# Performance work log

Hardware: AMD Instinct MI355X
Metric: run time of the kernel (lower is better)

Reference implementation:

```python
import jax, jax.numpy as jnp
import numpy as np

N_USERS = 100000
N_ITEMS = 50000
N_NODES = N_USERS + N_ITEMS
N_EDGES = 10000000
DIM = 64
N_LAYERS = 3


def setup_inputs() -> dict:
    key = jax.random.key(0)
    k1, k2, k3, k4, k5, k6, k7 = jax.random.split(key, 7)
    users = jax.random.randint(k1, (8192,), 0, N_USERS, dtype=jnp.int64 if jax.config.jax_enable_x64 else jnp.int32)
    items = jax.random.randint(k2, (8192,), 0, N_ITEMS, dtype=users.dtype)
    edge_src = jax.random.randint(k3, (N_EDGES,), 0, N_NODES, dtype=users.dtype)
    edge_dst = jax.random.randint(k4, (N_EDGES,), 0, N_NODES, dtype=users.dtype)
    edge_vals = jax.random.uniform(k5, (N_EDGES,), dtype=jnp.float32)
    user_emb = 0.1 * jax.random.normal(k6, (N_USERS, DIM), dtype=jnp.float32)
    item_emb = 0.1 * jax.random.normal(k7, (N_ITEMS, DIM), dtype=jnp.float32)
    return {"users": users, "items": items, "edge_src": edge_src,
            "edge_dst": edge_dst, "edge_vals": edge_vals,
            "user_emb": user_emb, "item_emb": item_emb}


def _spmm(edge_src, edge_dst, edge_vals, x):
    # y[dst] += vals * x[src]  (COO SpMM, edge-parallel)
    msgs = edge_vals[:, None] * x[edge_src]          # [E, D]
    return jax.ops.segment_sum(msgs, edge_dst, num_segments=N_NODES)


def _compute(edge_src, edge_dst, edge_vals, user_emb, item_emb):
    all_emds = jnp.concatenate([user_emb, item_emb], axis=0)  # [N, D]
    acc = all_emds
    cur = all_emds
    for _ in range(N_LAYERS):
        cur = _spmm(edge_src, edge_dst, edge_vals, cur)
        acc = acc + cur
    lgn_out = acc / jnp.asarray(N_LAYERS + 1, dtype=acc.dtype)  # mean over stacked layers
    return lgn_out[:N_USERS], lgn_out[N_USERS:]


def reference(users, items, edge_src, edge_dst, edge_vals, user_emb, item_emb):
    all_users, all_items = _compute(edge_src, edge_dst, edge_vals, user_emb, item_emb)
    users_embs = all_users[users]   # [B, D]
    items_embs = all_items[items]   # [B, D]
    gamma = jnp.sum(users_embs * items_embs, axis=1)  # [B]
    return gamma
```

## Files before the change

kernel.cpp:

```cpp
#include <hip/hip_runtime.h>

#define DIM 64
#define BROWS 512
#define LNB 512
#define TILE 8192
#define PMAXE 40960

typedef unsigned short bf16_t;

typedef int      iv4 __attribute__((ext_vector_type(4)));
typedef float    fv4 __attribute__((ext_vector_type(4)));
typedef unsigned uv4 __attribute__((ext_vector_type(4)));

__device__ __forceinline__ float bf2f_lo(unsigned u) {
    return __uint_as_float(u << 16);
}
__device__ __forceinline__ float bf2f_hi(unsigned u) {
    return __uint_as_float(u & 0xFFFF0000u);
}
__device__ __forceinline__ unsigned short f2bf(float f) {
    unsigned u = __float_as_uint(f);
    u += 0x7FFFu + ((u >> 16) & 1u);
    return (unsigned short)(u >> 16);
}
__device__ __forceinline__ unsigned pack2(float lo, float hi) {
    return (unsigned)f2bf(lo) | ((unsigned)f2bf(hi) << 16);
}

__device__ __forceinline__ unsigned enc_val14(float v) {
    float s = v * 16384.f + 0.5f;
    int u = (int)s;
    if (u > 16383) u = 16383;
    if (u < 0) u = 0;
    return (unsigned)u;
}
#define DEC_VAL14(p) ((float)((p) >> 18) * 6.103515625e-05f)
#define SRC_OF(p)    ((p) & 0x3FFFFu)

__global__ void build_xb(const float4* __restrict__ ue, const float4* __restrict__ ie,
                         ushort4* __restrict__ xb, long nU4, long total4) {
    long i = (long)blockIdx.x * blockDim.x + threadIdx.x;
    if (i >= total4) return;
    float4 v = (i < nU4) ? ue[i] : ie[i - nU4];
    ushort4 o;
    o.x = f2bf(v.x); o.y = f2bf(v.y); o.z = f2bf(v.z); o.w = f2bf(v.w);
    xb[i] = o;
}

__global__ void gather_accum_f32_2(const int* __restrict__ users, const int* __restrict__ items,
                                   const float* __restrict__ ue, const float* __restrict__ ie,
                                   float* __restrict__ accU, float* __restrict__ accI, int B) {
    long gid = (long)blockIdx.x * blockDim.x + threadIdx.x;
    int lane = (int)(gid & 15);
    long g = gid >> 4;
    if (g >= 2 * (long)B) return;
    const int* idx = (g < B) ? users : items;
    const float* x = (g < B) ? ue : ie;
    float* acc = (g < B) ? accU : accI;
    long b = (g < B) ? g : g - B;
    long node = (long)idx[b];
    float4 r = ((const float4*)(x + node * DIM))[lane];
    float4* a = (float4*)(acc + b * DIM) + lane;
    float4 av = *a;
    av.x += r.x; av.y += r.y; av.z += r.z; av.w += r.w;
    *a = av;
}

__global__ void gather_accum_bf16_2(const int* __restrict__ users, const int* __restrict__ items,
                                    int nU, const bf16_t* __restrict__ xb,
                                    float* __restrict__ accU, float* __restrict__ accI, int B) {
    long gid = (long)blockIdx.x * blockDim.x + threadIdx.x;
    int lane = (int)(gid & 7);
    long g = gid >> 3;
    if (g >= 2 * (long)B) return;
    long b;
    long node;
    float* acc;
    if (g < B) { b = g;     node = (long)users[b];      acc = accU; }
    else       { b = g - B; node = (long)items[b] + nU; acc = accI; }
    int4 r = *(const int4*)(xb + node * DIM + lane * 8);
    float4* ap = (float4*)(acc + b * DIM + lane * 8);
    float4 a0 = ap[0], a1 = ap[1];
    a0.x += bf2f_lo(r.x); a0.y += bf2f_hi(r.x);
    a0.z += bf2f_lo(r.y); a0.w += bf2f_hi(r.y);
    a1.x += bf2f_lo(r.z); a1.y += bf2f_hi(r.z);
    a1.z += bf2f_lo(r.w); a1.w += bf2f_hi(r.w);
    ap[0] = a0; ap[1] = a1;
}

__global__ void dot_pairs(const float* __restrict__ aU, const float* __restrict__ aI,
                          float* __restrict__ out, int B) {
    long gid = (long)blockIdx.x * blockDim.x + threadIdx.x;
    int lane = (int)(gid & 15);
    long b = gid >> 4;
    if (b >= B) return;
    float4 u = ((const float4*)(aU + b * DIM))[lane];
    float4 v = ((const float4*)(aI + b * DIM))[lane];
    float s = u.x * v.x + u.y * v.y + u.z * v.z + u.w * v.w;
    s += __shfl_xor(s, 1);
    s += __shfl_xor(s, 2);
    s += __shfl_xor(s, 4);
    s += __shfl_xor(s, 8);
    if (lane == 0) out[b] = s * (1.0f / 16.0f);
}

__global__ __launch_bounds__(1024) void bucket_hist(const int* __restrict__ edst,
                                                    int* __restrict__ bcnt, int E, int NB) {
    __shared__ int h[LNB];
    for (int i = threadIdx.x; i < NB; i += 1024) h[i] = 0;
    __syncthreads();
    int base = blockIdx.x * TILE;
    int end = base + TILE; if (end > E) end = E;
    int e = base + threadIdx.x * 4;
    for (; e + 3 < end; e += 4096) {
        iv4 d = __builtin_nontemporal_load((const iv4*)(edst + e));
        atomicAdd(&h[d.x >> 9], 1);
        atomicAdd(&h[d.y >> 9], 1);
        atomicAdd(&h[d.z >> 9], 1);
        atomicAdd(&h[d.w >> 9], 1);
    }
    for (; e < end; ++e)
        atomicAdd(&h[edst[e] >> 9], 1);
    __syncthreads();
    for (int i = threadIdx.x; i < NB; i += 1024)
        if (h[i]) atomicAdd(&bcnt[i], h[i]);
}

__global__ void scan_buckets(const int* __restrict__ bcnt, int* __restrict__ bptr,
                             int* __restrict__ bcur, int NB) {
    __shared__ int tmp[1024];
    int i = threadIdx.x;
    int v = (i < NB) ? bcnt[i] : 0;
    tmp[i] = v;
    __syncthreads();
    for (int off = 1; off < 1024; off <<= 1) {
        int t = (i >= off) ? tmp[i - off] : 0;
        __syncthreads();
        tmp[i] += t;
        __syncthreads();
    }
    if (i < NB) {
        int inc = tmp[i];
        bptr[i + 1] = inc;
        bcur[i] = inc - v;
        if (i == 0) bptr[0] = 0;
    }
}

__global__ void scan_block(const int* __restrict__ cnt, int* __restrict__ out,
                           int* __restrict__ blockSums, int n) {
    __shared__ int tmp[256];
    int i = blockIdx.x * 256 + threadIdx.x;
    int v = (i < n) ? cnt[i] : 0;
    tmp[threadIdx.x] = v;
    __syncthreads();
    for (int off = 1; off < 256; off <<= 1) {
        int t = (threadIdx.x >= off) ? tmp[threadIdx.x - off] : 0;
        __syncthreads();
        tmp[threadIdx.x] += t;
        __syncthreads();
    }
    if (i < n) out[i] = tmp[threadIdx.x];
    if (threadIdx.x == 255) blockSums[blockIdx.x] = tmp[255];
}

__global__ void scan_sums(int* __restrict__ blockSums, int nb) {
    __shared__ int tmp[1024];
    int i = threadIdx.x;
    tmp[i] = (i < nb) ? blockSums[i] : 0;
    __syncthreads();
    for (int off = 1; off < 1024; off <<= 1) {
        int t = (i >= off) ? tmp[i - off] : 0;
        __syncthreads();
        tmp[i] += t;
        __syncthreads();
    }
    if (i < nb) blockSums[i] = (i > 0) ? tmp[i - 1] : 0;
}

__global__ void scan_finalize(const int* __restrict__ cnt, const int* __restrict__ blockSums,
                              int* __restrict__ outp, int* __restrict__ start, int n) {
    int i = blockIdx.x * 256 + threadIdx.x;
    if (i >= n) return;
    int inc = outp[i + 1] + blockSums[blockIdx.x];
    outp[i + 1] = inc;
    start[i] = inc - cnt[i];
    if (i == 0) outp[0] = 0;
}

__global__ __launch_bounds__(1024) void bucket_scatter(
        const int* __restrict__ esrc, const int* __restrict__ edst,
        const float* __restrict__ evals, int* __restrict__ bcur,
        unsigned* __restrict__ tmpw, unsigned short* __restrict__ tmpd,
        int E, int NB) {
    __shared__ int h[LNB];
    __shared__ int cb[LNB];
    __shared__ int lofs[LNB];
    __shared__ unsigned sw[TILE];
    __shared__ unsigned short sd[TILE];
    const int tid = threadIdx.x;
    for (int i = tid; i < NB; i += 1024) h[i] = 0;
    __syncthreads();
    int base = blockIdx.x * TILE;
    int end = base + TILE; if (end > E) end = E;
    int e = base + tid * 4;
    for (; e + 3 < end; e += 4096) {
        iv4 d = __builtin_nontemporal_load((const iv4*)(edst + e));
        atomicAdd(&h[d.x >> 9], 1);
        atomicAdd(&h[d.y >> 9], 1);
        atomicAdd(&h[d.z >> 9], 1);
        atomicAdd(&h[d.w >> 9], 1);
    }
    for (; e < end; ++e)
        atomicAdd(&h[edst[e] >> 9], 1);
    __syncthreads();
    if (tid < LNB) lofs[tid] = (tid < NB) ? h[tid] : 0;
    __syncthreads();
    for (int off = 1; off < LNB; off <<= 1) {
        int t = (tid < LNB && tid >= off) ? lofs[tid - off] : 0;
        __syncthreads();
        if (tid < LNB) lofs[tid] += t;
        __syncthreads();
    }
    if (tid < NB) {
        int c = h[tid];
        cb[tid] = c ? atomicAdd(&bcur[tid], c) : 0;
    }
    __syncthreads();
    if (tid < NB) h[tid] = 0;
    __syncthreads();
    e = base + tid * 4;
    for (; e + 3 < end; e += 4096) {
        iv4 d4 = __builtin_nontemporal_load((const iv4*)(edst + e));
        iv4 s4 = __builtin_nontemporal_load((const iv4*)(esrc + e));
        fv4 v4 = __builtin_nontemporal_load((const fv4*)(evals + e));
        #pragma unroll
        for (int k = 0; k < 4; ++k) {
            int d = (k == 0) ? d4.x : (k == 1) ? d4.y : (k == 2) ? d4.z : d4.w;
            int s = (k == 0) ? s4.x : (k == 1) ? s4.y : (k == 2) ? s4.z : s4.w;
            float v = (k == 0) ? v4.x : (k == 1) ? v4.y : (k == 2) ? v4.z : v4.w;
            int b = d >> 9;
            int r = atomicAdd(&h[b], 1);
            int idx = (b ? lofs[b - 1] : 0) + r;
            sw[idx] = (unsigned)s | (enc_val14(v) << 18);
            sd[idx] = (unsigned short)(d & 511);
        }
    }
    for (; e < end; ++e) {
        int d = edst[e];
        int s = esrc[e];
        float v = evals[e];
        int b = d >> 9;
        int r = atomicAdd(&h[b], 1);
        int idx = (b ? lofs[b - 1] : 0) + r;
        sw[idx] = (unsigned)s | (enc_val14(v) << 18);
        sd[idx] = (unsigned short)(d & 511);
    }
    __syncthreads();
    int wid = tid >> 6;
    int lane = tid & 63;
    for (int b = wid; b < NB; b += 16) {
        int c = h[b];
        if (!c) continue;
        int sb = b ? lofs[b - 1] : 0;
        int gb = cb[b];
        for (int k = lane; k < c; k += 64) {
            tmpw[gb + k] = sw[sb + k];
            tmpd[gb + k] = sd[sb + k];
        }
    }
}

__device__ __forceinline__ void csr_hist_scan_rowptr(
        const unsigned short* __restrict__ tmpd, int beg, int end,
        int* lcnt, int* lofs, int* __restrict__ rowptr, int rbase, int N, int b, int NB) {
    const int T = 1024;
    if (threadIdx.x < BROWS) lcnt[threadIdx.x] = 0;
    __syncthreads();
    for (int e = beg + threadIdx.x; e < end; e += T) {
        int dl = __builtin_nontemporal_load(tmpd + e);
        atomicAdd(&lcnt[dl], 1);
    }
    __syncthreads();
    if (threadIdx.x < BROWS) lofs[threadIdx.x] = lcnt[threadIdx.x];
    __syncthreads();
    for (int off = 1; off < BROWS; off <<= 1) {
        int t = (threadIdx.x < BROWS && threadIdx.x >= off) ? lofs[threadIdx.x - off] : 0;
        __syncthreads();
        if (threadIdx.x < BROWS) lofs[threadIdx.x] += t;
        __syncthreads();
    }
    if (threadIdx.x < BROWS) {
        int r = rbase + threadIdx.x;
        if (r < N) rowptr[r] = beg + (threadIdx.x ? lofs[threadIdx.x - 1] : 0);
    }
    if (b == NB - 1 && threadIdx.x == 0) rowptr[N] = end;
    if (threadIdx.x < BROWS) lcnt[threadIdx.x] = 0;
    __syncthreads();
}

__global__ __launch_bounds__(1024) void csr_from_buckets_perm(
        const int* __restrict__ bptr, const unsigned* __restrict__ tmpw,
        const unsigned short* __restrict__ tmpd,
        unsigned* __restrict__ pairs, int* __restrict__ rowptr, int N, int NB) {
    extern __shared__ unsigned short perm[];
    __shared__ int lcnt[BROWS];
    __shared__ int lofs[BROWS];
    const int T = 1024;
    int b = blockIdx.x;
    int beg = bptr[b], end = bptr[b + 1];
    int cnt = end - beg;
    csr_hist_scan_rowptr(tmpd, beg, end, lcnt, lofs, rowptr, b * BROWS, N, b, NB);
    if (cnt <= PMAXE) {
        for (int e = beg + threadIdx.x; e < end; e += T) {
            int dl = __builtin_nontemporal_load(tmpd + e);
            int r = atomicAdd(&lcnt[dl], 1);
            int j = (dl ? lofs[dl - 1] : 0) + r;
            perm[j] = (unsigned short)(e - beg);
        }
        __syncthreads();
        for (int j = threadIdx.x; j < cnt; j += T)
            pairs[beg + j] = tmpw[beg + (int)perm[j]];
    } else {
        for (int e = beg + threadIdx.x; e < end; e += T) {
            unsigned w = tmpw[e];
            int dl = tmpd[e];
            int r = atomicAdd(&lcnt[dl], 1);
            pairs[beg + (dl ? lofs[dl - 1] : 0) + r] = w;
        }
    }
}

__global__ void csr_from_buckets(const int* __restrict__ bptr, const unsigned* __restrict__ tmpw,
                                 const unsigned short* __restrict__ tmpd,
                                 unsigned* __restrict__ pairs, int* __restrict__ rowptr,
                                 int N, int NB) {
    __shared__ int lcnt[BROWS];
    __shared__ int lofs[BROWS];
    const int T = 1024;
    int b = blockIdx.x;
    int beg = bptr[b], end = bptr[b + 1];
    csr_hist_scan_rowptr(tmpd, beg, end, lcnt, lofs, rowptr, b * BROWS, N, b, NB);
    for (int e = beg + threadIdx.x; e < end; e += T) {
        unsigned w = __builtin_nontemporal_load(tmpw + e);
        int dl = __builtin_nontemporal_load(tmpd + e);
        int r = atomicAdd(&lcnt[dl], 1);
        int basep = beg + (dl ? lofs[dl - 1] : 0);
        pairs[basep + r] = w;
    }
}

__global__ void count_deg(const int* __restrict__ dst, int* __restrict__ cnt, int E) {
    int e = blockIdx.x * blockDim.x + threadIdx.x;
    if (e >= E) return;
    atomicAdd(&cnt[dst[e]], 1);
}

__global__ void csr_fill(const int* __restrict__ src, const int* __restrict__ dst,
                         const float* __restrict__ vals, int* __restrict__ cursor,
                         unsigned* __restrict__ pairs, int E) {
    int e = blockIdx.x * blockDim.x + threadIdx.x;
    if (e >= E) return;
    int d = dst[e];
    int pos = atomicAdd(&cursor[d], 1);
    pairs[pos] = (unsigned)src[e] | (enc_val14(vals[e]) << 18);
}

template<int U>
__device__ __forceinline__ void spmm_body(const unsigned* pw, const bf16_t* __restrict__ xb,
                                          int lane, float* a) {
    int4 rr[U];
    #pragma unroll
    for (int k = 0; k < U; ++k)
        rr[k] = *(const int4*)(xb + (long)SRC_OF(pw[k]) * DIM + lane * 8);
    #pragma unroll
    for (int k = 0; k < U; ++k) {
        float v = DEC_VAL14(pw[k]);
        a[0] += v * bf2f_lo(rr[k].x); a[1] += v * bf2f_hi(rr[k].x);
        a[2] += v * bf2f_lo(rr[k].y); a[3] += v * bf2f_hi(rr[k].y);
        a[4] += v * bf2f_lo(rr[k].z); a[5] += v * bf2f_hi(rr[k].z);
        a[6] += v * bf2f_lo(rr[k].w); a[7] += v * bf2f_hi(rr[k].w);
    }
}

__device__ __forceinline__ void spmm_row(const unsigned* __restrict__ pairs, int beg, int end,
                                         const bf16_t* __restrict__ xb, int lane, float* a) {
    int e = beg;
    for (; e < end && (e & 3); ++e) {
        unsigned p = __builtin_nontemporal_load(pairs + e);
        spmm_body<1>(&p, xb, lane, a);
    }
    for (; e + 7 < end; e += 8) {
        uv4 w0 = __builtin_nontemporal_load((const uv4*)(pairs + e));
        uv4 w1 = __builtin_nontemporal_load((const uv4*)(pairs + e + 4));
        unsigned pw[8] = {w0.x, w0.y, w0.z, w0.w, w1.x, w1.y, w1.z, w1.w};
        spmm_body<8>(pw, xb, lane, a);
    }
    if (e + 3 < end) {
        uv4 w0 = __builtin_nontemporal_load((const uv4*)(pairs + e));
        unsigned pw[4] = {w0.x, w0.y, w0.z, w0.w};
        spmm_body<4>(pw, xb, lane, a);
        e += 4;
    }
    for (; e < end; ++e) {
        unsigned p = __builtin_nontemporal_load(pairs + e);
        spmm_body<1>(&p, xb, lane, a);
    }
}

__global__ void spmm_pull_bf16(const int* __restrict__ rowptr, const unsigned* __restrict__ pairs,
                               const bf16_t* __restrict__ xb, bf16_t* __restrict__ yb, int Nrows) {
    long gid = (long)blockIdx.x * blockDim.x + threadIdx.x;
    int lane = (int)(gid & 7);
    long r = gid >> 3;
    if (r >= Nrows) return;
    int beg = rowptr[r];
    int end = rowptr[r + 1];
    float a[8] = {0.f, 0.f, 0.f, 0.f, 0.f, 0.f, 0.f, 0.f};
    spmm_row(pairs, beg, end, xb, lane, a);
    int4 o;
    o.x = (int)pack2(a[0], a[1]);
    o.y = (int)pack2(a[2], a[3]);
    o.z = (int)pack2(a[4], a[5]);
    o.w = (int)pack2(a[6], a[7]);
    *(int4*)(yb + r * DIM + lane * 8) = o;
}

__global__ void spmm_rows_accum_fused(const int* __restrict__ users, const int* __restrict__ items,
                                      int nU, const int* __restrict__ rowptr,
                                      const unsigned* __restrict__ pairs, const bf16_t* __restrict__ xb,
                                      float* __restrict__ accU, float* __restrict__ accI, int B) {
    long gid = (long)blockIdx.x * blockDim.x + threadIdx.x;
    int lane = (int)(gid & 7);
    long g = gid >> 3;
    if (g >= 2 * (long)B) return;
    long b;
    long row;
    float* acc;
    if (g < B) { b = g;     row = (long)users[b];      acc = accU; }
    else       { b = g - B; row = (long)items[b] + nU; acc = accI; }
    int beg = rowptr[row];
    int end = rowptr[row + 1];
    int4 rs = *(const int4*)(xb + row * DIM + lane * 8);
    float a[8] = { bf2f_lo(rs.x), bf2f_hi(rs.x), bf2f_lo(rs.y), bf2f_hi(rs.y),
                   bf2f_lo(rs.z), bf2f_hi(rs.z), bf2f_lo(rs.w), bf2f_hi(rs.w) };
    spmm_row(pairs, beg, end, xb, lane, a);
    float4* ap = (float4*)(acc + b * DIM + lane * 8);
    float4 x0 = ap[0], x1 = ap[1];
    x0.x += a[0]; x0.y += a[1]; x0.z += a[2]; x0.w += a[3];
    x1.x += a[4]; x1.y += a[5]; x1.z += a[6]; x1.w += a[7];
    ap[0] = x0; ap[1] = x1;
}

extern "C" void kernel_launch(void* const* d_in, const int* in_sizes, int n_in,
                              void* d_out, int out_size, void* d_ws, size_t ws_size,
                              hipStream_t stream) {
    const int*   users = (const int*)d_in[0];
    const int*   items = (const int*)d_in[1];
    const int*   esrc  = (const int*)d_in[2];
    const int*   edst  = (const int*)d_in[3];
    const float* evals = (const float*)d_in[4];
    const float* uemb  = (const float*)d_in[5];
    const float* iemb  = (const float*)d_in[6];

    const int B  = in_sizes[0];
    const int E  = in_sizes[2];
    const int nU = in_sizes[5] / DIM;
    const int nI = in_sizes[6] / DIM;
    const int N  = nU + nI;
    const int NB = (N + BROWS - 1) / BROWS;

    const int T = 256;
    float* gout = (float*)d_out;

    static const bool perm_ok = []() {
        return hipFuncSetAttribute(
                   reinterpret_cast<const void*>(csr_from_buckets_perm),
                   hipFuncAttributeMaxDynamicSharedMemorySize,
                   PMAXE * (int)sizeof(unsigned short)) == hipSuccess;
    }();

    char* p = (char*)d_ws;
    float*  accU  = (float*)p;          p += (size_t)B * DIM * 4;
    float*  accI  = (float*)p;          p += (size_t)B * DIM * 4;
    bf16_t* xbCur = (bf16_t*)p;         p += (size_t)N * DIM * 2;
    bf16_t* xbNxt = (bf16_t*)p;         p += (size_t)N * DIM * 2;
    int*    rowptr = (int*)p;           p += (size_t)(N + 1) * 4;
    int*    bcnt   = (int*)p;           p += (size_t)NB * 4;
    int*    bptr   = (int*)p;           p += (size_t)(NB + 1) * 4;
    int*    bcur   = (int*)p;           p += (size_t)NB * 4;
    int*    blockSums = (int*)p;        p += 1024 * 4;
    int*    cnt    = (int*)p;           p += (size_t)N * 4;
    int*    cursor = (int*)p;           p += (size_t)N * 4;
    p = (char*)(((size_t)p + 15) & ~(size_t)15);
    unsigned* pairs = (unsigned*)p;     p += (size_t)E * 4;
    p = (char*)(((size_t)p + 15) & ~(size_t)15);
    size_t need_fb = (size_t)(p - (char*)d_ws);
    unsigned* tmpw = (unsigned*)p;      p += (size_t)E * 4;
    p = (char*)(((size_t)p + 15) & ~(size_t)15);
    unsigned short* tmpd = (unsigned short*)p; p += (size_t)E * 2;
    size_t need_fast = (size_t)(p - (char*)d_ws);
    (void)need_fb;

    long total4 = (long)N * (DIM / 4);
    long nU4    = (long)nU * (DIM / 4);
    int gb32 = (int)(((long)B * 32 + T - 1) / T);
    int gb16 = (int)(((long)B * 16 + T - 1) / T);
    int eb = (E + T - 1) / T;

    hipMemsetAsync(accU, 0, (size_t)B * DIM * 2 * sizeof(float), stream);
    gather_accum_f32_2<<<gb32, T, 0, stream>>>(users, items, uemb, iemb, accU, accI, B);

    build_xb<<<(int)((total4 + T - 1) / T), T, 0, stream>>>(
        (const float4*)uemb, (const float4*)iemb, (ushort4*)xbCur, nU4, total4);

    if (ws_size >= need_fast && NB <= LNB && N <= (1 << 18)) {
        int tb = (E + TILE - 1) / TILE;
        hipMemsetAsync(bcnt, 0, (size_t)NB * sizeof(int), stream);
        bucket_hist<<<tb, 1024, 0, stream>>>(edst, bcnt, E, NB);
        scan_buckets<<<1, 1024, 0, stream>>>(bcnt, bptr, bcur, NB);
        bucket_scatter<<<tb, 1024, 0, stream>>>(esrc, edst, evals, bcur, tmpw, tmpd, E, NB);
        if (perm_ok) {
            csr_from_buckets_perm<<<NB, 1024, PMAXE * sizeof(unsigned short), stream>>>(
                bptr, tmpw, tmpd, pairs, rowptr, N, NB);
        } else {
            csr_from_buckets<<<NB, 1024, 0, stream>>>(bptr, tmpw, tmpd, pairs, rowptr, N, NB);
        }
    } else {
        hipMemsetAsync(cnt, 0, (size_t)N * sizeof(int), stream);
        count_deg<<<eb, T, 0, stream>>>(edst, cnt, E);
        int nbN = (N + 255) / 256;
        scan_block<<<nbN, 256, 0, stream>>>(cnt, rowptr + 1, blockSums, N);
        scan_sums<<<1, 1024, 0, stream>>>(blockSums, nbN);
        scan_finalize<<<nbN, 256, 0, stream>>>(cnt, blockSums, rowptr, cursor, N);
        csr_fill<<<eb, T, 0, stream>>>(esrc, edst, evals, cursor, pairs, E);
    }

    int pb8 = (int)(((long)N * 8 + T - 1) / T);
    spmm_pull_bf16<<<pb8, T, 0, stream>>>(rowptr, pairs, xbCur, xbNxt, N);
    gather_accum_bf16_2<<<gb16, T, 0, stream>>>(users, items, nU, xbNxt, accU, accI, B);
    spmm_pull_bf16<<<pb8, T, 0, stream>>>(rowptr, pairs, xbNxt, xbCur, N);

    spmm_rows_accum_fused<<<gb16, T, 0, stream>>>(users, items, nU, rowptr, pairs, xbCur,
                                                  accU, accI, B);

    dot_pairs<<<gb16, T, 0, stream>>>(accU, accI, gout, B);
}
```

Before: 753.3 us.

## Quantize node embeddings to int8 with per-row scale for SpMM gathers

```diff
diff --git a/kernel.cpp b/kernel.cpp
--- a/kernel.cpp
+++ b/kernel.cpp
@@ -11,21 +11,6 @@
 typedef int      iv4 __attribute__((ext_vector_type(4)));
 typedef float    fv4 __attribute__((ext_vector_type(4)));
 typedef unsigned uv4 __attribute__((ext_vector_type(4)));
-
-__device__ __forceinline__ float bf2f_lo(unsigned u) {
-    return __uint_as_float(u << 16);
-}
-__device__ __forceinline__ float bf2f_hi(unsigned u) {
-    return __uint_as_float(u & 0xFFFF0000u);
-}
-__device__ __forceinline__ unsigned short f2bf(float f) {
-    unsigned u = __float_as_uint(f);
-    u += 0x7FFFu + ((u >> 16) & 1u);
-    return (unsigned short)(u >> 16);
-}
-__device__ __forceinline__ unsigned pack2(float lo, float hi) {
-    return (unsigned)f2bf(lo) | ((unsigned)f2bf(hi) << 16);
-}
 
 __device__ __forceinline__ unsigned enc_val14(float v) {
     float s = v * 16384.f + 0.5f;
@@ -37,14 +22,56 @@
 #define DEC_VAL14(p) ((float)((p) >> 18) * 6.103515625e-05f)
 #define SRC_OF(p)    ((p) & 0x3FFFFu)
 
-__global__ void build_xb(const float4* __restrict__ ue, const float4* __restrict__ ie,
-                         ushort4* __restrict__ xb, long nU4, long total4) {
-    long i = (long)blockIdx.x * blockDim.x + threadIdx.x;
-    if (i >= total4) return;
-    float4 v = (i < nU4) ? ue[i] : ie[i - nU4];
-    ushort4 o;
-    o.x = f2bf(v.x); o.y = f2bf(v.y); o.z = f2bf(v.z); o.w = f2bf(v.w);
-    xb[i] = o;
+__device__ __forceinline__ void quant_store_row(const float* a, int lane,
+                                                unsigned char* __restrict__ xq,
+                                                float* __restrict__ sc, long row) {
+    float m = 0.f;
+    #pragma unroll
+    for (int k = 0; k < 8; ++k) m = fmaxf(m, fabsf(a[k]));
+    m = fmaxf(m, __shfl_xor(m, 1));
+    m = fmaxf(m, __shfl_xor(m, 2));
+    m = fmaxf(m, __shfl_xor(m, 4));
+    float inv = (m > 0.f) ? 127.f / m : 0.f;
+    unsigned w0 = 0, w1 = 0;
+    #pragma unroll
+    for (int k = 0; k < 4; ++k) {
+        int q = (int)rintf(a[k] * inv);
+        w0 |= ((unsigned)(q & 0xFF)) << (8 * k);
+    }
+    #pragma unroll
+    for (int k = 0; k < 4; ++k) {
+        int q = (int)rintf(a[4 + k] * inv);
+        w1 |= ((unsigned)(q & 0xFF)) << (8 * k);
+    }
+    uint2 o; o.x = w0; o.y = w1;
+    *(uint2*)(xq + row * DIM + lane * 8) = o;
+    if (lane == 0) sc[row] = m * (1.0f / 127.0f);
+}
+
+__device__ __forceinline__ void dec8_accum(uint2 r, float v, float* a) {
+    unsigned x = r.x, y = r.y;
+    a[0] += v * (float)(((int)(x << 24)) >> 24);
+    a[1] += v * (float)(((int)(x << 16)) >> 24);
+    a[2] += v * (float)(((int)(x <<  8)) >> 24);
+    a[3] += v * (float)(((int)x) >> 24);
+    a[4] += v * (float)(((int)(y << 24)) >> 24);
+    a[5] += v * (float)(((int)(y << 16)) >> 24);
+    a[6] += v * (float)(((int)(y <<  8)) >> 24);
+    a[7] += v * (float)(((int)y) >> 24);
+}
+
+__global__ void build_xb_q8(const float* __restrict__ ue, const float* __restrict__ ie,
+                            unsigned char* __restrict__ xq, float* __restrict__ sc,
+                            int nU, int N) {
+    long gid = (long)blockIdx.x * blockDim.x + threadIdx.x;
+    int lane = (int)(gid & 7);
+    long r = gid >> 3;
+    if (r >= N) return;
+    const float* srcp = (r < nU) ? (ue + r * DIM) : (ie + (r - nU) * DIM);
+    float4 f0 = ((const float4*)srcp)[lane * 2];
+    float4 f1 = ((const float4*)srcp)[lane * 2 + 1];
+    float a[8] = {f0.x, f0.y, f0.z, f0.w, f1.x, f1.y, f1.z, f1.w};
+    quant_store_row(a, lane, xq, sc, r);
 }
 
 __global__ void gather_accum_f32_2(const int* __restrict__ users, const int* __restrict__ items,
@@ -66,9 +93,10 @@
     *a = av;
 }
 
-__global__ void gather_accum_bf16_2(const int* __restrict__ users, const int* __restrict__ items,
-                                    int nU, const bf16_t* __restrict__ xb,
-                                    float* __restrict__ accU, float* __restrict__ accI, int B) {
+__global__ void gather_accum_q8_2(const int* __restrict__ users, const int* __restrict__ items,
+                                  int nU, const unsigned char* __restrict__ xq,
+                                  const float* __restrict__ xs,
+                                  float* __restrict__ accU, float* __restrict__ accI, int B) {
     long gid = (long)blockIdx.x * blockDim.x + threadIdx.x;
     int lane = (int)(gid & 7);
     long g = gid >> 3;
@@ -78,13 +106,14 @@
     float* acc;
     if (g < B) { b = g;     node = (long)users[b];      acc = accU; }
     else       { b = g - B; node = (long)items[b] + nU; acc = accI; }
-    int4 r = *(const int4*)(xb + node * DIM + lane * 8);
+    uint2 r = *(const uint2*)(xq + node * DIM + lane * 8);
+    float s = xs[node];
+    float a[8] = {0.f, 0.f, 0.f, 0.f, 0.f, 0.f, 0.f, 0.f};
+    dec8_accum(r, s, a);
     float4* ap = (float4*)(acc + b * DIM + lane * 8);
     float4 a0 = ap[0], a1 = ap[1];
-    a0.x += bf2f_lo(r.x); a0.y += bf2f_hi(r.x);
-    a0.z += bf2f_lo(r.y); a0.w += bf2f_hi(r.y);
-    a1.x += bf2f_lo(r.z); a1.y += bf2f_hi(r.z);
-    a1.z += bf2f_lo(r.w); a1.w += bf2f_hi(r.w);
+    a0.x += a[0]; a0.y += a[1]; a0.z += a[2]; a0.w += a[3];
+    a1.x += a[4]; a1.y += a[5]; a1.z += a[6]; a1.w += a[7];
     ap[0] = a0; ap[1] = a1;
 }
 
@@ -367,49 +396,51 @@
 }
 
 template<int U>
-__device__ __forceinline__ void spmm_body(const unsigned* pw, const bf16_t* __restrict__ xb,
-                                          int lane, float* a) {
-    int4 rr[U];
+__device__ __forceinline__ void spmm_body(const unsigned* pw,
+                                          const unsigned char* __restrict__ xq,
+                                          const float* __restrict__ xs, int lane, float* a) {
+    uint2 rr[U];
+    float vs[U];
+    #pragma unroll
+    for (int k = 0; k < U; ++k) {
+        long s = (long)SRC_OF(pw[k]);
+        rr[k] = *(const uint2*)(xq + s * DIM + lane * 8);
+        vs[k] = DEC_VAL14(pw[k]) * xs[s];
+    }
     #pragma unroll
     for (int k = 0; k < U; ++k)
-        rr[k] = *(const int4*)(xb + (long)SRC_OF(pw[k]) * DIM + lane * 8);
-    #pragma unroll
-    for (int k = 0; k < U; ++k) {
-        float v = DEC_VAL14(pw[k]);
-        a[0] += v * bf2f_lo(rr[k].x); a[1] += v * bf2f_hi(rr[k].x);
-        a[2] += v * bf2f_lo(rr[k].y); a[3] += v * bf2f_hi(rr[k].y);
-        a[4] += v * bf2f_lo(rr[k].z); a[5] += v * bf2f_hi(rr[k].z);
-        a[6] += v * bf2f_lo(rr[k].w); a[7] += v * bf2f_hi(rr[k].w);
-    }
+        dec8_accum(rr[k], vs[k], a);
 }
 
 __device__ __forceinline__ void spmm_row(const unsigned* __restrict__ pairs, int beg, int end,
-                                         const bf16_t* __restrict__ xb, int lane, float* a) {
+                                         const unsigned char* __restrict__ xq,
+                                         const float* __restrict__ xs, int lane, float* a) {
     int e = beg;
     for (; e < end && (e & 3); ++e) {
         unsigned p = __builtin_nontemporal_load(pairs + e);
-        spmm_body<1>(&p, xb, lane, a);
+        spmm_body<1>(&p, xq, xs, lane, a);
     }
     for (; e + 7 < end; e += 8) {
         uv4 w0 = __builtin_nontemporal_load((const uv4*)(pairs + e));
         uv4 w1 = __builtin_nontemporal_load((const uv4*)(pairs + e + 4));
         unsigned pw[8] = {w0.x, w0.y, w0.z, w0.w, w1.x, w1.y, w1.z, w1.w};
-        spmm_body<8>(pw, xb, lane, a);
+        spmm_body<8>(pw, xq, xs, lane, a);
     }
     if (e + 3 < end) {
         uv4 w0 = __builtin_nontemporal_load((const uv4*)(pairs + e));
         unsigned pw[4] = {w0.x, w0.y, w0.z, w0.w};
-        spmm_body<4>(pw, xb, lane, a);
+        spmm_body<4>(pw, xq, xs, lane, a);
         e += 4;
     }
     for (; e < end; ++e) {
         unsigned p = __builtin_nontemporal_load(pairs + e);
-        spmm_body<1>(&p, xb, lane, a);
-    }
-}
-
-__global__ void spmm_pull_bf16(const int* __restrict__ rowptr, const unsigned* __restrict__ pairs,
-                               const bf16_t* __restrict__ xb, bf16_t* __restrict__ yb, int Nrows) {
+        spmm_body<1>(&p, xq, xs, lane, a);
+    }
+}
+
+__global__ void spmm_pull_q8(const int* __restrict__ rowptr, const unsigned* __restrict__ pairs,
+                             const unsigned char* __restrict__ xq, const float* __restrict__ xs,
+                             unsigned char* __restrict__ yq, float* __restrict__ ys, int Nrows) {
     long gid = (long)blockIdx.x * blockDim.x + threadIdx.x;
     int lane = (int)(gid & 7);
     long r = gid >> 3;
@@ -417,18 +448,15 @@
     int beg = rowptr[r];
     int end = rowptr[r + 1];
     float a[8] = {0.f, 0.f, 0.f, 0.f, 0.f, 0.f, 0.f, 0.f};
-    spmm_row(pairs, beg, end, xb, lane, a);
-    int4 o;
-    o.x = (int)pack2(a[0], a[1]);
-    o.y = (int)pack2(a[2], a[3]);
-    o.z = (int)pack2(a[4], a[5]);
-    o.w = (int)pack2(a[6], a[7]);
-    *(int4*)(yb + r * DIM + lane * 8) = o;
+    spmm_row(pairs, beg, end, xq, xs, lane, a);
+    quant_store_row(a, lane, yq, ys, r);
 }
 
 __global__ void spmm_rows_accum_fused(const int* __restrict__ users, const int* __restrict__ items,
                                       int nU, const int* __restrict__ rowptr,
-                                      const unsigned* __restrict__ pairs, const bf16_t* __restrict__ xb,
+                                      const unsigned* __restrict__ pairs,
+                                      const unsigned char* __restrict__ xq,
+                                      const float* __restrict__ xs,
                                       float* __restrict__ accU, float* __restrict__ accI, int B) {
     long gid = (long)blockIdx.x * blockDim.x + threadIdx.x;
     int lane = (int)(gid & 7);
@@ -441,10 +469,10 @@
     else       { b = g - B; row = (long)items[b] + nU; acc = accI; }
     int beg = rowptr[row];
     int end = rowptr[row + 1];
-    int4 rs = *(const int4*)(xb + row * DIM + lane * 8);
-    float a[8] = { bf2f_lo(rs.x), bf2f_hi(rs.x), bf2f_lo(rs.y), bf2f_hi(rs.y),
-                   bf2f_lo(rs.z), bf2f_hi(rs.z), bf2f_lo(rs.w), bf2f_hi(rs.w) };
-    spmm_row(pairs, beg, end, xb, lane, a);
+    float a[8] = {0.f, 0.f, 0.f, 0.f, 0.f, 0.f, 0.f, 0.f};
+    uint2 rs = *(const uint2*)(xq + row * DIM + lane * 8);
+    dec8_accum(rs, xs[row], a);
+    spmm_row(pairs, beg, end, xq, xs, lane, a);
     float4* ap = (float4*)(acc + b * DIM + lane * 8);
     float4 x0 = ap[0], x1 = ap[1];
     x0.x += a[0]; x0.y += a[1]; x0.z += a[2]; x0.w += a[3];
@@ -483,8 +511,11 @@
     char* p = (char*)d_ws;
     float*  accU  = (float*)p;          p += (size_t)B * DIM * 4;
     float*  accI  = (float*)p;          p += (size_t)B * DIM * 4;
-    bf16_t* xbCur = (bf16_t*)p;         p += (size_t)N * DIM * 2;
-    bf16_t* xbNxt = (bf16_t*)p;         p += (size_t)N * DIM * 2;
+    unsigned char* xqCur = (unsigned char*)p;  p += (size_t)N * DIM;
+    unsigned char* xqNxt = (unsigned char*)p;  p += (size_t)N * DIM;
+    p = (char*)(((size_t)p + 15) & ~(size_t)15);
+    float*  scCur = (float*)p;          p += (size_t)N * 4;
+    float*  scNxt = (float*)p;          p += (size_t)N * 4;
     int*    rowptr = (int*)p;           p += (size_t)(N + 1) * 4;
     int*    bcnt   = (int*)p;           p += (size_t)NB * 4;
     int*    bptr   = (int*)p;           p += (size_t)(NB + 1) * 4;
@@ -502,8 +533,6 @@
     size_t need_fast = (size_t)(p - (char*)d_ws);
     (void)need_fb;
 
-    long total4 = (long)N * (DIM / 4);
-    long nU4    = (long)nU * (DIM / 4);
     int gb32 = (int)(((long)B * 32 + T - 1) / T);
     int gb16 = (int)(((long)B * 16 + T - 1) / T);
     int eb = (E + T - 1) / T;
@@ -511,8 +540,8 @@
     hipMemsetAsync(accU, 0, (size_t)B * DIM * 2 * sizeof(float), stream);
     gather_accum_f32_2<<<gb32, T, 0, stream>>>(users, items, uemb, iemb, accU, accI, B);
 
-    build_xb<<<(int)((total4 + T - 1) / T), T, 0, stream>>>(
-        (const float4*)uemb, (const float4*)iemb, (ushort4*)xbCur, nU4, total4);
+    int qb8 = (int)(((long)N * 8 + T - 1) / T);
+    build_xb_q8<<<qb8, T, 0, stream>>>(uemb, iemb, xqCur, scCur, nU, N);
 
     if (ws_size >= need_fast && NB <= LNB && N <= (1 << 18)) {
         int tb = (E + TILE - 1) / TILE;
@@ -537,12 +566,12 @@
     }
 
     int pb8 = (int)(((long)N * 8 + T - 1) / T);
-    spmm_pull_bf16<<<pb8, T, 0, stream>>>(rowptr, pairs, xbCur, xbNxt, N);
-    gather_accum_bf16_2<<<gb16, T, 0, stream>>>(users, items, nU, xbNxt, accU, accI, B);
-    spmm_pull_bf16<<<pb8, T, 0, stream>>>(rowptr, pairs, xbNxt, xbCur, N);
-
-    spmm_rows_accum_fused<<<gb16, T, 0, stream>>>(users, items, nU, rowptr, pairs, xbCur,
-                                                  accU, accI, B);
+    spmm_pull_q8<<<pb8, T, 0, stream>>>(rowptr, pairs, xqCur, scCur, xqNxt, scNxt, N);
+    gather_accum_q8_2<<<gb16, T, 0, stream>>>(users, items, nU, xqNxt, scNxt, accU, accI, B);
+    spmm_pull_q8<<<pb8, T, 0, stream>>>(rowptr, pairs, xqNxt, scNxt, xqCur, scCur, N);
+
+    spmm_rows_accum_fused<<<gb16, T, 0, stream>>>(users, items, nU, rowptr, pairs,
+                                                  xqCur, scCur, accU, accI, B);
 
     dot_pairs<<<gb16, T, 0, stream>>>(accU, accI, gout, B);
 }
```

Result: slower. 775.0 us (+2.9%).
